# Kernel tuning notes

Hardware: AMD Instinct MI355X
Metric: run time of the kernel (lower is better)

Reference implementation:

```python
import jax, jax.numpy as jnp
import numpy as np

N_BLOCKS = 4
DIN = 4000      # features per input block
DE = 128        # embed dims per block
DLAT = 512      # latent dim per block
ALPHA = 0.3     # Keras LeakyReLU default negative slope


def setup_inputs() -> dict:
    key = jax.random.key(0)
    ks = jax.random.split(key, 7)
    N = 4096
    x = jax.random.normal(ks[0], (N, N_BLOCKS * DIN), dtype=jnp.float32)
    mask = jax.random.bernoulli(ks[1], 0.5, (N, N_BLOCKS * DIN))
    embed = jax.random.normal(ks[2], (N, N_BLOCKS * DE), dtype=jnp.float32)
    batches = jax.random.normal(ks[3], (N, 8), dtype=jnp.float32)
    mean_vals = jax.random.normal(ks[4], (N_BLOCKS * DIN,), dtype=jnp.float32)
    fan_in = DIN + DE + 8
    W = jax.random.normal(ks[5], (N_BLOCKS, fan_in, DLAT), dtype=jnp.float32) / np.sqrt(fan_in)
    b = jnp.zeros((N_BLOCKS, DLAT), dtype=jnp.float32)
    return {"x": x, "mask": mask, "embed": embed, "batches": batches,
            "mean_vals": mean_vals, "W": W, "b": b}


def reference(x, mask, embed, batches, mean_vals, W, b):
    N = x.shape[0]
    db = batches.shape[1]
    # masked mean-centering: x = where(mask, x - mean, 0)
    xm = jnp.where(mask, x - mean_vals[None, :], jnp.zeros((), x.dtype))
    # equal-sized splits == reshape into [N, B, din] / [N, B, de]
    xb = xm.reshape(N, N_BLOCKS, DIN)
    eb = embed.reshape(N, N_BLOCKS, DE)
    bb = jnp.broadcast_to(batches[:, None, :], (N, N_BLOCKS, db))
    inp = jnp.concatenate([xb, eb, bb], axis=-1)  # [N, B, DIN+DE+db]
    h = jnp.einsum('nbi,bio->nbo', inp, W) + b[None, :, :]  # grouped GEMM
    h = jnp.where(h >= 0, h, ALPHA * h)  # LeakyReLU(alpha=0.3)
    return h.reshape(N, N_BLOCKS * DLAT)  # concat of per-block outputs
```

## Files before the change

### kernel.cpp

```cpp
#include <hip/hip_runtime.h>

#define NROWS 4096
#define NBLK 4
#define DIN 4000
#define DE 128
#define DB 8
#define DLAT 512
#define FANIN 4136
#define KPAD 4224
#define NKT 66
#define XC 16000
#define OUTC 2048
#define TC 192

typedef __attribute__((ext_vector_type(8))) short short8;
typedef __attribute__((ext_vector_type(4))) float floatx4;

__device__ __forceinline__ unsigned short f2bf(float f) {
    unsigned int u = __builtin_bit_cast(unsigned int, f);
    u = (u + 0x7FFFu + ((u >> 16) & 1u)) >> 16;
    return (unsigned short)u;
}

__device__ __forceinline__ void async16(const void* g, void* l) {
    __builtin_amdgcn_global_load_lds(
        (const __attribute__((address_space(1))) void*)g,
        (__attribute__((address_space(3))) void*)l, 16, 0, 0);
}

__global__ void prep_w(const float* __restrict__ W, unsigned short* __restrict__ Wp) {
    int tid = blockIdx.x * 256 + threadIdx.x;
    int n  = tid & 511;
    int t2 = tid >> 9;
    int kc = t2 % 528;
    int b  = t2 / 528;
    unsigned short outv[8];
#pragma unroll
    for (int j = 0; j < 8; ++j) {
        int pk = kc * 8 + j;
        float v = 0.f;
        int wr = -1;
        if (pk < DIN) wr = pk;
        else if (pk >= 4032 && pk < 4168) wr = pk - 32;
        if (wr >= 0) v = W[((size_t)b * FANIN + wr) * DLAT + n];
        outv[j] = f2bf(v);
    }
    *reinterpret_cast<short8*>(Wp + ((size_t)(b * DLAT + n) * KPAD + kc * 8)) =
        *reinterpret_cast<const short8*>(outv);
}

__global__ void prep_t(const float* __restrict__ embed, const float* __restrict__ batches,
                       unsigned short* __restrict__ T) {
    int i  = blockIdx.x * 256 + threadIdx.x;
    int t  = i % TC;
    int nb = i / TC;
    int b  = nb & 3;
    int n  = nb >> 2;
    float v = 0.f;
    if (t < DE)            v = embed[(size_t)n * (NBLK * DE) + b * DE + t];
    else if (t < DE + DB)  v = batches[(size_t)n * DB + (t - DE)];
    T[i] = f2bf(v);
}

__global__ __launch_bounds__(1024, 4) void gemm_k(
    const float* __restrict__ x, const int* __restrict__ mask,
    const float* __restrict__ mean, const float* __restrict__ bias,
    const unsigned short* __restrict__ Wp, const unsigned short* __restrict__ T,
    float* __restrict__ out) {
    __shared__ unsigned short Asm_[128 * 64];
    __shared__ unsigned short Bsm_[256 * 64];

    int bid = blockIdx.x;
    int nt  = bid & 1;
    int mt  = (bid >> 1) & 31;
    int b   = bid >> 6;
    int tid  = threadIdx.x;
    int lane = tid & 63;
    int w    = tid >> 6;
    int wm   = w >> 2;
    int wn   = w & 3;
    int quad = lane >> 4;
    int l16  = lane & 15;
    int row0 = mt * 128;

    floatx4 acc[2][4];
#pragma unroll
    for (int m = 0; m < 2; ++m)
#pragma unroll
        for (int n2 = 0; n2 < 4; ++n2) acc[m][n2] = (floatx4){0.f, 0.f, 0.f, 0.f};

    for (int kt = 0; kt < NKT; ++kt) {
        if (kt < 63) {
#pragma unroll
            for (int i = 0; i < 2; ++i) {
                int c  = i * 1024 + tid;
                int r  = c >> 4;
                int c4 = (c & 15) << 2;
                int col = kt * 64 + c4;
                int rg  = row0 + r;
                float4 v = make_float4(0.f, 0.f, 0.f, 0.f);
                if (col < DIN) {
                    size_t gi = (size_t)rg * XC + b * DIN + col;
                    float4 xv = *reinterpret_cast<const float4*>(x + gi);
                    int4   mv = *reinterpret_cast<const int4*>(mask + gi);
                    float4 me = *reinterpret_cast<const float4*>(mean + (b * DIN + col));
                    v.x = mv.x ? xv.x - me.x : 0.f;
                    v.y = mv.y ? xv.y - me.y : 0.f;
                    v.z = mv.z ? xv.z - me.z : 0.f;
                    v.w = mv.w ? xv.w - me.w : 0.f;
                }
                ushort4 pk;
                pk.x = f2bf(v.x); pk.y = f2bf(v.y); pk.z = f2bf(v.z); pk.w = f2bf(v.w);
                *reinterpret_cast<ushort4*>(&Asm_[r * 64 + c4]) = pk;
            }
        } else {
            int r = tid >> 3, k16 = tid & 7;
            int rg = row0 + r;
            const unsigned short* src =
                T + (((size_t)rg * NBLK + b) * TC + (kt - 63) * 64 + k16 * 8);
            async16(src, &Asm_[tid * 8]);
        }
#pragma unroll
        for (int i = 0; i < 2; ++i) {
            int c = i * 1024 + tid;
            int nl = c >> 3, k16 = c & 7;
            const unsigned short* src =
                Wp + ((size_t)(b * DLAT + nt * 256 + nl) * KPAD + kt * 64 + k16 * 8);
            async16(src, &Bsm_[c * 8]);
        }
        __syncthreads();
#pragma unroll
        for (int s = 0; s < 2; ++s) {
            short8 af[2], bfr[4];
#pragma unroll
            for (int m = 0; m < 2; ++m)
                af[m] = *reinterpret_cast<const short8*>(
                    &Asm_[(wm * 32 + m * 16 + l16) * 64 + s * 32 + quad * 8]);
#pragma unroll
            for (int n2 = 0; n2 < 4; ++n2)
                bfr[n2] = *reinterpret_cast<const short8*>(
                    &Bsm_[(wn * 64 + n2 * 16 + l16) * 64 + s * 32 + quad * 8]);
#pragma unroll
            for (int m = 0; m < 2; ++m)
#pragma unroll
                for (int n2 = 0; n2 < 4; ++n2)
                    acc[m][n2] = __builtin_amdgcn_mfma_f32_16x16x32_bf16(
                        af[m], bfr[n2], acc[m][n2], 0, 0, 0);
        }
        __syncthreads();
    }

#pragma unroll
    for (int m = 0; m < 2; ++m) {
#pragma unroll
        for (int n2 = 0; n2 < 4; ++n2) {
            int col_l = wn * 64 + n2 * 16 + l16;
            int gcol  = nt * 256 + col_l;
            float bv = bias[b * DLAT + gcol];
#pragma unroll
            for (int r = 0; r < 4; ++r) {
                int row_l = wm * 32 + m * 16 + quad * 4 + r;
                float v = acc[m][n2][r] + bv;
                v = v >= 0.f ? v : 0.3f * v;
                out[(size_t)(row0 + row_l) * OUTC + b * DLAT + gcol] = v;
            }
        }
    }
}

extern "C" void kernel_launch(void* const* d_in, const int* in_sizes, int n_in,
                              void* d_out, int out_size, void* d_ws, size_t ws_size,
                              hipStream_t stream) {
    const float* x       = (const float*)d_in[0];
    const int*   mask    = (const int*)d_in[1];
    const float* embed   = (const float*)d_in[2];
    const float* batches = (const float*)d_in[3];
    const float* mean    = (const float*)d_in[4];
    const float* W       = (const float*)d_in[5];
    const float* bias    = (const float*)d_in[6];
    float* out = (float*)d_out;

    unsigned short* Wp = (unsigned short*)d_ws;
    unsigned short* T  = Wp + (size_t)NBLK * DLAT * KPAD;

    prep_w<<<dim3(4224), dim3(256), 0, stream>>>(W, Wp);
    prep_t<<<dim3(12288), dim3(256), 0, stream>>>(embed, batches, T);
    gemm_k<<<dim3(256), dim3(1024), 0, stream>>>(x, mask, mean, bias, Wp, T, out);
}
```

Baseline: 714.0 us.

## Retile GEMM to 128x128 with 256 threads, XOR-swizzled LDS, and tiled W transpose

The GEMM now uses 256-thread blocks, each computing a 128x128 output tile with a 4x4 MFMA accumulator per wave, launched as 512 blocks instead of 256. The A and B tiles in shared memory use an XOR swizzle to reduce bank conflicts on fragment reads. The weight-prep kernel now stages through shared memory, giving coalesced float4 reads of W and a transposed write. Each block issues fewer loads per MFMA, at the cost of more registers per thread and lower occupancy.

```diff
diff --git a/kernel.cpp b/kernel.cpp
--- a/kernel.cpp
+++ b/kernel.cpp
@@ -29,24 +29,40 @@
 }
 
 __global__ void prep_w(const float* __restrict__ W, unsigned short* __restrict__ Wp) {
-    int tid = blockIdx.x * 256 + threadIdx.x;
-    int n  = tid & 511;
-    int t2 = tid >> 9;
-    int kc = t2 % 528;
-    int b  = t2 / 528;
-    unsigned short outv[8];
-#pragma unroll
-    for (int j = 0; j < 8; ++j) {
-        int pk = kc * 8 + j;
-        float v = 0.f;
-        int wr = -1;
-        if (pk < DIN) wr = pk;
-        else if (pk >= 4032 && pk < 4168) wr = pk - 32;
-        if (wr >= 0) v = W[((size_t)b * FANIN + wr) * DLAT + n];
-        outv[j] = f2bf(v);
-    }
-    *reinterpret_cast<short8*>(Wp + ((size_t)(b * DLAT + n) * KPAD + kc * 8)) =
-        *reinterpret_cast<const short8*>(outv);
+    __shared__ unsigned short tile[64 * 68];
+    int bid = blockIdx.x;
+    int nt = bid & 7;
+    int t2 = bid >> 3;
+    int kt = t2 % 66;
+    int b  = t2 / 66;
+    int tid = threadIdx.x;
+    int n0 = nt * 64;
+    int k0 = kt * 64;
+#pragma unroll
+    for (int i = 0; i < 4; ++i) {
+        int c = i * 256 + tid;
+        int r = c >> 4;
+        int q = (c & 15) * 4;
+        int pk = k0 + r;
+        int wr = (pk < DIN) ? pk : ((pk >= 4032 && pk < 4168) ? pk - 32 : -1);
+        float4 v = make_float4(0.f, 0.f, 0.f, 0.f);
+        if (wr >= 0)
+            v = *reinterpret_cast<const float4*>(W + ((size_t)b * FANIN + wr) * DLAT + n0 + q);
+        ushort4 u4 = make_ushort4(f2bf(v.x), f2bf(v.y), f2bf(v.z), f2bf(v.w));
+        *reinterpret_cast<ushort4*>(&tile[r * 68 + q]) = u4;
+    }
+    __syncthreads();
+#pragma unroll
+    for (int i = 0; i < 2; ++i) {
+        int c = i * 256 + tid;
+        int nl = c >> 3;
+        int kc = c & 7;
+        unsigned short o[8];
+#pragma unroll
+        for (int j = 0; j < 8; ++j) o[j] = tile[(kc * 8 + j) * 68 + nl];
+        *reinterpret_cast<short8*>(Wp + ((size_t)(b * DLAT + n0 + nl)) * KPAD + k0 + kc * 8) =
+            *reinterpret_cast<const short8*>(o);
+    }
 }
 
 __global__ void prep_t(const float* __restrict__ embed, const float* __restrict__ batches,
@@ -62,107 +78,125 @@
     T[i] = f2bf(v);
 }
 
-__global__ __launch_bounds__(1024, 4) void gemm_k(
+__global__ __launch_bounds__(256, 3) void gemm_k(
     const float* __restrict__ x, const int* __restrict__ mask,
     const float* __restrict__ mean, const float* __restrict__ bias,
     const unsigned short* __restrict__ Wp, const unsigned short* __restrict__ T,
     float* __restrict__ out) {
     __shared__ unsigned short Asm_[128 * 64];
-    __shared__ unsigned short Bsm_[256 * 64];
+    __shared__ unsigned short Bsm_[128 * 64];
 
     int bid = blockIdx.x;
-    int nt  = bid & 1;
-    int mt  = (bid >> 1) & 31;
-    int b   = bid >> 6;
+    int nt  = bid & 3;
+    int b   = (bid >> 2) & 3;
+    int mt  = bid >> 4;
     int tid  = threadIdx.x;
     int lane = tid & 63;
     int w    = tid >> 6;
-    int wm   = w >> 2;
-    int wn   = w & 3;
+    int wm   = w >> 1;
+    int wn   = w & 1;
     int quad = lane >> 4;
     int l16  = lane & 15;
     int row0 = mt * 128;
-
-    floatx4 acc[2][4];
-#pragma unroll
-    for (int m = 0; m < 2; ++m)
-#pragma unroll
-        for (int n2 = 0; n2 < 4; ++n2) acc[m][n2] = (floatx4){0.f, 0.f, 0.f, 0.f};
+    int n0   = nt * 128;
+
+    floatx4 acc[4][4];
+#pragma unroll
+    for (int m = 0; m < 4; ++m)
+#pragma unroll
+        for (int n = 0; n < 4; ++n) acc[m][n] = (floatx4){0.f, 0.f, 0.f, 0.f};
 
     for (int kt = 0; kt < NKT; ++kt) {
         if (kt < 63) {
 #pragma unroll
-            for (int i = 0; i < 2; ++i) {
-                int c  = i * 1024 + tid;
-                int r  = c >> 4;
-                int c4 = (c & 15) << 2;
-                int col = kt * 64 + c4;
-                int rg  = row0 + r;
-                float4 v = make_float4(0.f, 0.f, 0.f, 0.f);
+            for (int i = 0; i < 4; ++i) {
+                int c  = i * 256 + tid;
+                int r  = c >> 3;
+                int cg = c & 7;
+                int col = kt * 64 + cg * 8;
+                short8 v8 = (short8){0, 0, 0, 0, 0, 0, 0, 0};
                 if (col < DIN) {
-                    size_t gi = (size_t)rg * XC + b * DIN + col;
-                    float4 xv = *reinterpret_cast<const float4*>(x + gi);
-                    int4   mv = *reinterpret_cast<const int4*>(mask + gi);
-                    float4 me = *reinterpret_cast<const float4*>(mean + (b * DIN + col));
-                    v.x = mv.x ? xv.x - me.x : 0.f;
-                    v.y = mv.y ? xv.y - me.y : 0.f;
-                    v.z = mv.z ? xv.z - me.z : 0.f;
-                    v.w = mv.w ? xv.w - me.w : 0.f;
+                    size_t gi = (size_t)(row0 + r) * XC + (size_t)b * DIN + col;
+                    const float4* xp = reinterpret_cast<const float4*>(x + gi);
+                    const int4*   mp = reinterpret_cast<const int4*>(mask + gi);
+                    const float4* ep = reinterpret_cast<const float4*>(mean + b * DIN + col);
+                    float4 x0 = xp[0], x1 = xp[1];
+                    int4   m0 = mp[0], m1 = mp[1];
+                    float4 e0 = ep[0], e1 = ep[1];
+                    float f0 = m0.x ? x0.x - e0.x : 0.f;
+                    float f1 = m0.y ? x0.y - e0.y : 0.f;
+                    float f2 = m0.z ? x0.z - e0.z : 0.f;
+                    float f3 = m0.w ? x0.w - e0.w : 0.f;
+                    float f4 = m1.x ? x1.x - e1.x : 0.f;
+                    float f5 = m1.y ? x1.y - e1.y : 0.f;
+                    float f6 = m1.z ? x1.z - e1.z : 0.f;
+                    float f7 = m1.w ? x1.w - e1.w : 0.f;
+                    v8 = (short8){(short)f2bf(f0), (short)f2bf(f1), (short)f2bf(f2),
+                                  (short)f2bf(f3), (short)f2bf(f4), (short)f2bf(f5),
+                                  (short)f2bf(f6), (short)f2bf(f7)};
                 }
-                ushort4 pk;
-                pk.x = f2bf(v.x); pk.y = f2bf(v.y); pk.z = f2bf(v.z); pk.w = f2bf(v.w);
-                *reinterpret_cast<ushort4*>(&Asm_[r * 64 + c4]) = pk;
+                *reinterpret_cast<short8*>(&Asm_[r * 64 + ((cg ^ (r & 7)) * 8)]) = v8;
             }
         } else {
-            int r = tid >> 3, k16 = tid & 7;
-            int rg = row0 + r;
+#pragma unroll
+            for (int i = 0; i < 4; ++i) {
+                int c  = i * 256 + tid;
+                int r  = c >> 3;
+                int cl = c & 7;
+                int cg = cl ^ (r & 7);
+                const unsigned short* src =
+                    T + ((size_t)(row0 + r) * NBLK + b) * TC + (kt - 63) * 64 + cg * 8;
+                async16(src, &Asm_[c * 8]);
+            }
+        }
+#pragma unroll
+        for (int i = 0; i < 4; ++i) {
+            int c  = i * 256 + tid;
+            int nl = c >> 3;
+            int cl = c & 7;
+            int cg = cl ^ (nl & 7);
             const unsigned short* src =
-                T + (((size_t)rg * NBLK + b) * TC + (kt - 63) * 64 + k16 * 8);
-            async16(src, &Asm_[tid * 8]);
-        }
-#pragma unroll
-        for (int i = 0; i < 2; ++i) {
-            int c = i * 1024 + tid;
-            int nl = c >> 3, k16 = c & 7;
-            const unsigned short* src =
-                Wp + ((size_t)(b * DLAT + nt * 256 + nl) * KPAD + kt * 64 + k16 * 8);
+                Wp + ((size_t)(b * DLAT + n0 + nl)) * KPAD + kt * 64 + cg * 8;
             async16(src, &Bsm_[c * 8]);
         }
         __syncthreads();
 #pragma unroll
         for (int s = 0; s < 2; ++s) {
-            short8 af[2], bfr[4];
-#pragma unroll
-            for (int m = 0; m < 2; ++m)
+            short8 af[4], bfr[4];
+#pragma unroll
+            for (int m = 0; m < 4; ++m) {
+                int ar = wm * 64 + m * 16 + l16;
                 af[m] = *reinterpret_cast<const short8*>(
-                    &Asm_[(wm * 32 + m * 16 + l16) * 64 + s * 32 + quad * 8]);
-#pragma unroll
-            for (int n2 = 0; n2 < 4; ++n2)
-                bfr[n2] = *reinterpret_cast<const short8*>(
-                    &Bsm_[(wn * 64 + n2 * 16 + l16) * 64 + s * 32 + quad * 8]);
-#pragma unroll
-            for (int m = 0; m < 2; ++m)
-#pragma unroll
-                for (int n2 = 0; n2 < 4; ++n2)
-                    acc[m][n2] = __builtin_amdgcn_mfma_f32_16x16x32_bf16(
-                        af[m], bfr[n2], acc[m][n2], 0, 0, 0);
+                    &Asm_[ar * 64 + (((s * 4 + quad) ^ (ar & 7)) * 8)]);
+            }
+#pragma unroll
+            for (int n = 0; n < 4; ++n) {
+                int br = wn * 64 + n * 16 + l16;
+                bfr[n] = *reinterpret_cast<const short8*>(
+                    &Bsm_[br * 64 + (((s * 4 + quad) ^ (br & 7)) * 8)]);
+            }
+#pragma unroll
+            for (int m = 0; m < 4; ++m)
+#pragma unroll
+                for (int n = 0; n < 4; ++n)
+                    acc[m][n] = __builtin_amdgcn_mfma_f32_16x16x32_bf16(
+                        af[m], bfr[n], acc[m][n], 0, 0, 0);
         }
         __syncthreads();
     }
 
 #pragma unroll
-    for (int m = 0; m < 2; ++m) {
-#pragma unroll
-        for (int n2 = 0; n2 < 4; ++n2) {
-            int col_l = wn * 64 + n2 * 16 + l16;
-            int gcol  = nt * 256 + col_l;
-            float bv = bias[b * DLAT + gcol];
+    for (int m = 0; m < 4; ++m) {
+#pragma unroll
+        for (int n = 0; n < 4; ++n) {
+            int col_l = wn * 64 + n * 16 + l16;
+            float bv = bias[b * DLAT + n0 + col_l];
 #pragma unroll
             for (int r = 0; r < 4; ++r) {
-                int row_l = wm * 32 + m * 16 + quad * 4 + r;
-                float v = acc[m][n2][r] + bv;
+                int row_l = wm * 64 + m * 16 + quad * 4 + r;
+                float v = acc[m][n][r] + bv;
                 v = v >= 0.f ? v : 0.3f * v;
-                out[(size_t)(row0 + row_l) * OUTC + b * DLAT + gcol] = v;
+                out[(size_t)(row0 + row_l) * OUTC + b * DLAT + n0 + col_l] = v;
             }
         }
     }
@@ -183,7 +217,7 @@
     unsigned short* Wp = (unsigned short*)d_ws;
     unsigned short* T  = Wp + (size_t)NBLK * DLAT * KPAD;
 
-    prep_w<<<dim3(4224), dim3(256), 0, stream>>>(W, Wp);
+    prep_w<<<dim3(2112), dim3(256), 0, stream>>>(W, Wp);
     prep_t<<<dim3(12288), dim3(256), 0, stream>>>(embed, batches, T);
-    gemm_k<<<dim3(256), dim3(1024), 0, stream>>>(x, mask, mean, bias, Wp, T, out);
-}
+    gemm_k<<<dim3(512), dim3(256), 0, stream>>>(x, mask, mean, bias, Wp, T, out);
+}
```

Result: slower. 749.6 us (+5.0%).
